# Kernel tuning notes

Measured on AMD Instinct MI355X. Metric: run time of the kernel, lower is better.

## Reference

```python
import jax, jax.numpy as jnp
import numpy as np

K = 3          # kernel size
STRIDE = 1
PAD = 1
GROUPS = 32    # GroupNorm groups
EPS = 1e-5


def setup_inputs() -> dict:
    key = jax.random.key(0)
    ks = jax.random.split(key, 6)
    B, Cin, H, W, Cout = 4, 256, 64, 64, 256
    K2 = K * K
    x = jax.random.normal(ks[0], (B, Cin, H, W), jnp.float32)
    offset = jax.random.normal(ks[1], (B, 2 * K2, H, W), jnp.float32)
    mask = jax.random.uniform(ks[2], (B, K2, H, W), jnp.float32)
    weight = jax.random.normal(ks[3], (Cout, Cin, K, K), jnp.float32) * (1.0 / np.sqrt(Cin * K2))
    bias = jnp.zeros((Cout,), jnp.float32)
    gamma = jnp.ones((Cout,), jnp.float32)   # constant_init(norm, 1)
    beta = jnp.zeros((Cout,), jnp.float32)   # bias=0
    return {"x": x, "offset": offset, "mask": mask, "weight": weight,
            "bias": bias, "gamma": gamma, "beta": beta}


def _modulated_deform_conv(x, offset, mask, weight, bias):
    """DCNv2: bilinear-sample x at learned offsets, modulate by mask, conv-accumulate."""
    B, Cin, H, W = x.shape
    Cout = weight.shape[0]
    K2 = K * K
    Ho = (H + 2 * PAD - K) // STRIDE + 1
    Wo = (W + 2 * PAD - K) // STRIDE + 1

    # base sampling grid per kernel point: [K2, Ho, Wo]
    ky, kx = jnp.meshgrid(jnp.arange(K), jnp.arange(K), indexing='ij')
    ky = ky.reshape(K2).astype(jnp.float32)
    kx = kx.reshape(K2).astype(jnp.float32)
    hs = (jnp.arange(Ho) * STRIDE - PAD).astype(jnp.float32)
    ws = (jnp.arange(Wo) * STRIDE - PAD).astype(jnp.float32)

    off = offset.reshape(B, K2, 2, Ho, Wo)  # interleaved (dy, dx) per kernel point
    y = ky[None, :, None, None] + hs[None, None, :, None] + off[:, :, 0]   # [B,K2,Ho,Wo]
    xc = kx[None, :, None, None] + ws[None, None, None, :] + off[:, :, 1]  # [B,K2,Ho,Wo]

    y0 = jnp.floor(y)
    x0 = jnp.floor(xc)
    dy = y - y0
    dx = xc - x0
    y0i = y0.astype(jnp.int32)
    x0i = x0.astype(jnp.int32)

    x_flat = x.reshape(B, Cin, H * W)

    def corner(yi, xi, w):
        # corner-wise zero padding outside the image (matches mmcv bilinear)
        valid = (yi >= 0) & (yi <= H - 1) & (xi >= 0) & (xi <= W - 1)
        idx = jnp.clip(yi, 0, H - 1) * W + jnp.clip(xi, 0, W - 1)  # [B,K2,Ho,Wo]
        idx_f = idx.reshape(B, -1)
        v = jax.vmap(lambda xf, i: xf[:, i])(x_flat, idx_f)  # [B, Cin, K2*Ho*Wo]
        wv = (w * valid.astype(w.dtype)).reshape(B, 1, -1)
        return v * wv

    val = (corner(y0i,     x0i,     (1 - dy) * (1 - dx))
         + corner(y0i,     x0i + 1, (1 - dy) * dx)
         + corner(y0i + 1, x0i,     dy * (1 - dx))
         + corner(y0i + 1, x0i + 1, dy * dx))
    val = val.reshape(B, Cin, K2, Ho, Wo) * mask[:, None]  # modulate

    w_r = weight.reshape(Cout, Cin, K2)
    out = jnp.einsum('bckhw,ock->bohw', val, w_r) + bias[None, :, None, None]
    return out


def _group_norm(x, gamma, beta):
    B, C, H, W = x.shape
    g = x.reshape(B, GROUPS, C // GROUPS, H, W)
    mu = g.mean(axis=(2, 3, 4), keepdims=True)
    var = ((g - mu) ** 2).mean(axis=(2, 3, 4), keepdims=True)
    g = (g - mu) * jax.lax.rsqrt(var + EPS)
    return g.reshape(B, C, H, W) * gamma[None, :, None, None] + beta[None, :, None, None]


def reference(x, offset, mask, weight, bias, gamma, beta):
    out = _modulated_deform_conv(x, offset, mask, weight, bias)
    out = _group_norm(out, gamma, beta)
    return jax.nn.relu(out)
```

## Files before the change

kernel.cpp:

```cpp
#include <hip/hip_runtime.h>
#include <math.h>

#define BB    4
#define CIN   256
#define HH    64
#define WWID  64
#define COUT  256
#define KKS   3
#define K2    9
#define PADV  1
#define HWSZ  4096
#define GROUPS 32
#define CPG   8
#define EPSV  1e-5f
#define NKC   36

typedef __attribute__((ext_vector_type(8))) short bf16x8;
typedef __attribute__((ext_vector_type(4))) float f32x4;
typedef __attribute__((ext_vector_type(2))) float f32x2;

__device__ __forceinline__ unsigned short f2bf(float f) {
    unsigned u = __float_as_uint(f);
    u = (u + 0x7fffu + ((u >> 16) & 1u)) >> 16;
    return (unsigned short)u;
}
__device__ __forceinline__ f32x2 up2(unsigned q) {
    f32x2 v;
    v.x = __uint_as_float(q << 16);
    v.y = __uint_as_float(q & 0xffff0000u);
    return v;
}
__device__ __forceinline__ unsigned cvtpk(f32x2 f) {
    unsigned r;
    asm("v_cvt_pk_bf16_f32 %0, %1, %2" : "=v"(r) : "v"(f.x), "v"(f.y));
    return r;
}

__global__ __launch_bounds__(256)
void k_pre(const float* __restrict__ x, unsigned short* __restrict__ xh,
           const float* __restrict__ w, unsigned short* __restrict__ wtb,
           float* __restrict__ gstat) {
    int t = threadIdx.x;
    if (blockIdx.x < 64) {
        __shared__ float tile[32][65];
        int hw0 = blockIdx.x * 64;
        int c0  = blockIdx.y * 32;
        int b   = blockIdx.z;
        const float* xp = x + (size_t)b * CIN * HWSZ;
        int col = t & 63, r0 = t >> 6;
        #pragma unroll
        for (int i = 0; i < 8; i++)
            tile[i * 4 + r0][col] = xp[(c0 + i * 4 + r0) * HWSZ + hw0 + col];
        __syncthreads();
        int hw = t >> 2, cq = t & 3;
        union { unsigned short s[8]; uint4 qq; } pk;
        #pragma unroll
        for (int k = 0; k < 8; k++) pk.s[k] = f2bf(tile[cq * 8 + k][hw]);
        *(uint4*)((char*)xh + (((size_t)b * HWSZ + hw0 + hw) * CIN + c0 + cq * 8) * 2) = pk.qq;
    } else {
        if (blockIdx.y == 0 && blockIdx.z == 0)
            for (int i = t; i < BB * GROUPS * 2 + 8; i += 256) gstat[i] = 0.f;
        int idx = (blockIdx.y * 4 + blockIdx.z) * 256 + t;
        int co = idx >> 5, c8 = idx & 31;
        int q  = c8 >> 3;
        int ks = (c8 & 7) >> 2;
        int hf = c8 & 3;
        int lane16 = hf * 16 + (co & 15);
        for (int k2 = 0; k2 < K2; k2++) {
            int kc = k2 * 4 + q;
            union { unsigned short s[8]; uint4 qq; } pk;
            #pragma unroll
            for (int j = 0; j < 8; j++)
                pk.s[j] = f2bf(w[(co * CIN + c8 * 8 + j) * K2 + k2]);
            size_t phys = (size_t)(((co >> 4) * 36 + kc)) * 2048 + ks * 1024 + lane16 * 16;
            *(uint4*)((char*)wtb + phys) = pk.qq;
        }
    }
}

#define GATHER2(garr, gwarr, kn) do { \
    int k2n_ = (kn) >> 2, qn_ = (kn) & 3; \
    int cb_ = (px0 * K2 + k2n_) * 4; \
    int4   ci_ = *(const int4*)&cidx[cb_]; \
    float4 cw_ = *(const float4*)&cwgt[cb_]; \
    gwarr[0] = cw_.x; gwarr[1] = cw_.y; gwarr[2] = cw_.z; gwarr[3] = cw_.w; \
    const char* xq_ = xb + qn_ * 128; \
    garr[0] = *(const uint4*)(xq_ + ci_.x); \
    garr[1] = *(const uint4*)(xq_ + ci_.y); \
    garr[2] = *(const uint4*)(xq_ + ci_.z); \
    garr[3] = *(const uint4*)(xq_ + ci_.w); \
} while (0)

#define ISSUE_A(Ar) do { \
    Ar[0] = *(const bf16x8*)(ap0);        Ar[1] = *(const bf16x8*)(ap0 + 1024); \
    Ar[2] = *(const bf16x8*)(ap1);        Ar[3] = *(const bf16x8*)(ap1 + 1024); \
    ap0 += 2048; ap1 += 2048; \
} while (0)

#define PACK(garr, gwarr, Bdst) do { \
    f32x2 f0 = {0.f, 0.f}, f1 = {0.f, 0.f}, f2 = {0.f, 0.f}, f3 = {0.f, 0.f}; \
    _Pragma("unroll") \
    for (int c_ = 0; c_ < 4; c_++) { \
        f32x2 wv_ = { gwarr[c_], gwarr[c_] }; \
        f0 = __builtin_elementwise_fma(wv_, up2(garr[c_].x), f0); \
        f1 = __builtin_elementwise_fma(wv_, up2(garr[c_].y), f1); \
        f2 = __builtin_elementwise_fma(wv_, up2(garr[c_].z), f2); \
        f3 = __builtin_elementwise_fma(wv_, up2(garr[c_].w), f3); \
    } \
    uint4 pk_; \
    pk_.x = cvtpk(f0); pk_.y = cvtpk(f1); pk_.z = cvtpk(f2); pk_.w = cvtpk(f3); \
    *(uint4*)&(Bdst)[bofs0] = pk_; \
} while (0)

#define MFMA_STEP(Ar, Bc) do { \
    __builtin_amdgcn_s_setprio(1); \
    _Pragma("unroll") \
    for (int ks_ = 0; ks_ < 2; ks_++) { \
        int up_ = ((ks_ * 4 + hf) ^ skey) * 8; \
        bf16x8 bv_[4]; \
        _Pragma("unroll") \
        for (int ni_ = 0; ni_ < 4; ni_++) \
            bv_[ni_] = *(const bf16x8*)&(Bc)[(ni_ * 16 + r16) * 64 + up_]; \
        _Pragma("unroll") \
        for (int mi_ = 0; mi_ < 2; mi_++) \
            _Pragma("unroll") \
            for (int ni_ = 0; ni_ < 4; ni_++) \
                acc[mi_][ni_] = __builtin_amdgcn_mfma_f32_16x16x32_bf16( \
                    Ar[mi_ * 2 + ks_], bv_[ni_], acc[mi_][ni_], 0, 0, 0); \
    } \
    __builtin_amdgcn_s_setprio(0); \
} while (0)

#define LGKM_BAR() do { \
    asm volatile("s_waitcnt lgkmcnt(0)\n\ts_barrier" ::: "memory"); \
    __builtin_amdgcn_sched_barrier(0); \
} while (0)

#define BODY(kc, Acur, Anxt, Bcur, Bnxt, gU, gwU, gF, gwF) do { \
    ISSUE_A(Anxt); \
    GATHER2(gF, gwF, (kc) + 2); \
    __builtin_amdgcn_sched_barrier(0); \
    MFMA_STEP(Acur, Bcur); \
    __builtin_amdgcn_sched_barrier(0); \
    PACK(gU, gwU, Bnxt); \
    LGKM_BAR(); \
} while (0)

__global__ __launch_bounds__(512, 2)
void k_conv(const unsigned short* __restrict__ wtb, const unsigned short* __restrict__ xh,
            const float* __restrict__ offset, const float* __restrict__ mask,
            const float* __restrict__ bias, float* __restrict__ out,
            float* __restrict__ gstat) {
    __shared__ __align__(16) unsigned short Bs[2][64 * 64];
    __shared__ __align__(16) int   cidx[64 * K2 * 4];
    __shared__ __align__(16) float cwgt[64 * K2 * 4];
    __shared__ float gs[32], gss[32];

    int lid = blockIdx.x;
    int strip = (lid & 7) * 32 + (lid >> 3);
    int b = strip >> 6;
    int hwbase = (strip & 63) * 64;

    int t = threadIdx.x, w = t >> 6, l = t & 63;
    int r16 = l & 15, hf = l >> 4;
    int skey = r16 & 7;

    if (t < 32) { gs[t] = 0.f; gss[t] = 0.f; }

    for (int i = t; i < 64 * K2; i += 512) {
        int px = i / K2, k2 = i - px * K2;
        int hw = hwbase + px;
        int ho = hw >> 6, wo = hw & 63;
        int ky = k2 / KKS, kx = k2 - ky * KKS;
        float dy = offset[((b * (2 * K2) + k2 * 2 + 0) * HWSZ) + hw];
        float dx = offset[((b * (2 * K2) + k2 * 2 + 1) * HWSZ) + hw];
        float m  = mask[(b * K2 + k2) * HWSZ + hw];
        float y  = (float)(ky + ho - PADV) + dy;
        float xc = (float)(kx + wo - PADV) + dx;
        float y0f = floorf(y), x0f = floorf(xc);
        float fy = y - y0f, fx = xc - x0f;
        int y0 = (int)y0f, x0 = (int)x0f;
        int   yy[2] = { y0, y0 + 1 };
        int   xx[2] = { x0, x0 + 1 };
        float wy[2] = { 1.f - fy, fy };
        float wx[2] = { 1.f - fx, fx };
        #pragma unroll
        for (int ii = 0; ii < 2; ii++)
            #pragma unroll
            for (int jj = 0; jj < 2; jj++) {
                int yi = yy[ii], xi = xx[jj];
                bool valid = (yi >= 0) && (yi < HH) && (xi >= 0) && (xi < WWID);
                int yc  = min(max(yi, 0), HH - 1);
                int xcc = min(max(xi, 0), WWID - 1);
                cidx[i * 4 + ii * 2 + jj] = (yc * WWID + xcc) << 9;
                cwgt[i * 4 + ii * 2 + jj] = valid ? (wy[ii] * wx[jj] * m) : 0.f;
            }
    }

    const char* wb = (const char*)wtb + (size_t)l * 16;
    const char* ap0 = wb + (size_t)((w * 2 + 0) * 36) * 2048;
    const char* ap1 = wb + (size_t)((w * 2 + 1) * 36) * 2048;

    int sc  = t & 7;
    int px0 = t >> 3;
    const char* xb = (const char*)xh + (size_t)b * HWSZ * CIN * 2 + sc * 16;
    int bofs0 = px0 * 64 + (sc ^ (px0 & 7)) * 8;

    f32x4 acc[2][4];
    #pragma unroll
    for (int mi = 0; mi < 2; mi++)
        #pragma unroll
        for (int ni = 0; ni < 4; ni++) acc[mi][ni] = (f32x4)0.f;

    __syncthreads();

    uint4 gA[4], gB[4]; float gwA[4], gwB[4];
    bf16x8 Aa[4], Ab[4];
    GATHER2(gA, gwA, 0);
    ISSUE_A(Aa);
    GATHER2(gB, gwB, 1);
    PACK(gA, gwA, Bs[0]);
    LGKM_BAR();

    unsigned short* Bs0 = &Bs[0][0];
    unsigned short* Bs1 = &Bs[1][0];

    for (int kc2 = 0; kc2 < 34; kc2 += 2) {
        BODY(kc2,     Aa, Ab, Bs0, Bs1, gB, gwB, gA, gwA);
        BODY(kc2 + 1, Ab, Aa, Bs1, Bs0, gA, gwA, gB, gwB);
    }
    ISSUE_A(Ab);
    __builtin_amdgcn_sched_barrier(0);
    MFMA_STEP(Aa, Bs0);
    __builtin_amdgcn_sched_barrier(0);
    PACK(gB, gwB, Bs1);
    LGKM_BAR();
    MFMA_STEP(Ab, Bs1);

    float s4[2] = {0,0}, ss4[2] = {0,0};
    #pragma unroll
    for (int mi = 0; mi < 2; mi++) {
        #pragma unroll
        for (int r = 0; r < 4; r++) {
            int co = w * 32 + mi * 16 + hf * 4 + r;
            float bs = bias[co];
            float* orow = out + ((size_t)(b * COUT + co)) * HWSZ;
            #pragma unroll
            for (int ni = 0; ni < 4; ni++) {
                int n = hwbase + ni * 16 + r16;
                float v = acc[mi][ni][r] + bs;
                orow[n] = v;
                s4[mi] += v; ss4[mi] += v * v;
            }
        }
    }
    int gb = hf >> 1;
    #pragma unroll
    for (int mi = 0; mi < 2; mi++) {
        atomicAdd(&gs [w * 4 + mi * 2 + gb], s4[mi]);
        atomicAdd(&gss[w * 4 + mi * 2 + gb], ss4[mi]);
    }
    __syncthreads();
    if (t < 32) {
        atomicAdd(&gstat[(b * GROUPS + t) * 2 + 0], gs[t]);
        atomicAdd(&gstat[(b * GROUPS + t) * 2 + 1], gss[t]);
    }
}

__global__ __launch_bounds__(256)
void k_gnfinal(float* __restrict__ out, const float* __restrict__ gstat,
               const float* __restrict__ gamma, const float* __restrict__ beta) {
    int i4 = blockIdx.x * 256 + threadIdx.x;
    int e  = i4 * 4;
    int c  = (e >> 12) & 255;
    int b  = e >> 20;
    int g  = c >> 3;
    float s  = gstat[((b * GROUPS) + g) * 2 + 0];
    float ss = gstat[((b * GROUPS) + g) * 2 + 1];
    const float inv = 1.f / (float)(CPG * HWSZ);
    float mu  = s * inv;
    float var = ss * inv - mu * mu;
    float rstd = rsqrtf(var + EPSV);
    float ga = gamma[c] * rstd;
    float be = beta[c] - mu * ga;
    float4 v = ((float4*)out)[i4];
    v.x = fmaxf(v.x * ga + be, 0.f);
    v.y = fmaxf(v.y * ga + be, 0.f);
    v.z = fmaxf(v.z * ga + be, 0.f);
    v.w = fmaxf(v.w * ga + be, 0.f);
    ((float4*)out)[i4] = v;
}

extern "C" void kernel_launch(void* const* d_in, const int* in_sizes, int n_in,
                              void* d_out, int out_size, void* d_ws, size_t ws_size,
                              hipStream_t stream) {
    const float* x      = (const float*)d_in[0];
    const float* offset = (const float*)d_in[1];
    const float* mask   = (const float*)d_in[2];
    const float* weight = (const float*)d_in[3];
    const float* bias   = (const float*)d_in[4];
    const float* gamma  = (const float*)d_in[5];
    const float* beta   = (const float*)d_in[6];
    float* out = (float*)d_out;

    unsigned short* xh    = (unsigned short*)d_ws;
    unsigned short* wtb   = xh + (size_t)4194304;
    float*          gstat = (float*)(wtb + (size_t)589824);

    k_pre<<<dim3(65, 8, 4), 256, 0, stream>>>(x, xh, weight, wtb, gstat);
    k_conv<<<256, 512, 0, stream>>>(wtb, xh, offset, mask, bias, out, gstat);
    k_gnfinal<<<(size_t)BB * COUT * HWSZ / 1024, 256, 0, stream>>>(out, gstat, gamma, beta);
}
```

Measured before the change: 134.4 us.

## Double K-chunk per pipeline stage to halve barriers and use nontemporal weight loads

```diff
diff --git a/kernel.cpp b/kernel.cpp
--- a/kernel.cpp
+++ b/kernel.cpp
@@ -13,7 +13,7 @@
 #define GROUPS 32
 #define CPG   8
 #define EPSV  1e-5f
-#define NKC   36
+#define NST   18
 
 typedef __attribute__((ext_vector_type(8))) short bf16x8;
 typedef __attribute__((ext_vector_type(4))) float f32x4;
@@ -91,13 +91,19 @@
     garr[3] = *(const uint4*)(xq_ + ci_.w); \
 } while (0)
 
-#define ISSUE_A(Ar) do { \
-    Ar[0] = *(const bf16x8*)(ap0);        Ar[1] = *(const bf16x8*)(ap0 + 1024); \
-    Ar[2] = *(const bf16x8*)(ap1);        Ar[3] = *(const bf16x8*)(ap1 + 1024); \
-    ap0 += 2048; ap1 += 2048; \
-} while (0)
-
-#define PACK(garr, gwarr, Bdst) do { \
+#define ISSUE_A8(Ar) do { \
+    Ar[0] = __builtin_nontemporal_load((const bf16x8*)(ap0)); \
+    Ar[1] = __builtin_nontemporal_load((const bf16x8*)(ap0 + 1024)); \
+    Ar[2] = __builtin_nontemporal_load((const bf16x8*)(ap0 + 2048)); \
+    Ar[3] = __builtin_nontemporal_load((const bf16x8*)(ap0 + 3072)); \
+    Ar[4] = __builtin_nontemporal_load((const bf16x8*)(ap1)); \
+    Ar[5] = __builtin_nontemporal_load((const bf16x8*)(ap1 + 1024)); \
+    Ar[6] = __builtin_nontemporal_load((const bf16x8*)(ap1 + 2048)); \
+    Ar[7] = __builtin_nontemporal_load((const bf16x8*)(ap1 + 3072)); \
+    ap0 += 4096; ap1 += 4096; \
+} while (0)
+
+#define PACK(garr, gwarr, Bdst, half) do { \
     f32x2 f0 = {0.f, 0.f}, f1 = {0.f, 0.f}, f2 = {0.f, 0.f}, f3 = {0.f, 0.f}; \
     _Pragma("unroll") \
     for (int c_ = 0; c_ < 4; c_++) { \
@@ -109,24 +115,24 @@
     } \
     uint4 pk_; \
     pk_.x = cvtpk(f0); pk_.y = cvtpk(f1); pk_.z = cvtpk(f2); pk_.w = cvtpk(f3); \
-    *(uint4*)&(Bdst)[bofs0] = pk_; \
+    *(uint4*)&(Bdst)[bofs0 + (half) * 64] = pk_; \
 } while (0)
 
 #define MFMA_STEP(Ar, Bc) do { \
     __builtin_amdgcn_s_setprio(1); \
     _Pragma("unroll") \
-    for (int ks_ = 0; ks_ < 2; ks_++) { \
+    for (int ks_ = 0; ks_ < 4; ks_++) { \
         int up_ = ((ks_ * 4 + hf) ^ skey) * 8; \
         bf16x8 bv_[4]; \
         _Pragma("unroll") \
         for (int ni_ = 0; ni_ < 4; ni_++) \
-            bv_[ni_] = *(const bf16x8*)&(Bc)[(ni_ * 16 + r16) * 64 + up_]; \
+            bv_[ni_] = *(const bf16x8*)&(Bc)[(ni_ * 16 + r16) * 128 + up_]; \
         _Pragma("unroll") \
         for (int mi_ = 0; mi_ < 2; mi_++) \
             _Pragma("unroll") \
             for (int ni_ = 0; ni_ < 4; ni_++) \
                 acc[mi_][ni_] = __builtin_amdgcn_mfma_f32_16x16x32_bf16( \
-                    Ar[mi_ * 2 + ks_], bv_[ni_], acc[mi_][ni_], 0, 0, 0); \
+                    Ar[mi_ * 4 + ks_], bv_[ni_], acc[mi_][ni_], 0, 0, 0); \
     } \
     __builtin_amdgcn_s_setprio(0); \
 } while (0)
@@ -136,13 +142,15 @@
     __builtin_amdgcn_sched_barrier(0); \
 } while (0)
 
-#define BODY(kc, Acur, Anxt, Bcur, Bnxt, gU, gwU, gF, gwF) do { \
-    ISSUE_A(Anxt); \
-    GATHER2(gF, gwF, (kc) + 2); \
+#define BODY(s, Acur, Anxt, Bcur, Bnxt, u0, uw0, u1, uw1, f0a, fw0, f1a, fw1) do { \
+    ISSUE_A8(Anxt); \
+    GATHER2(f0a, fw0, 2 * ((s) + 2)); \
+    GATHER2(f1a, fw1, 2 * ((s) + 2) + 1); \
     __builtin_amdgcn_sched_barrier(0); \
     MFMA_STEP(Acur, Bcur); \
     __builtin_amdgcn_sched_barrier(0); \
-    PACK(gU, gwU, Bnxt); \
+    PACK(u0, uw0, Bnxt, 0); \
+    PACK(u1, uw1, Bnxt, 1); \
     LGKM_BAR(); \
 } while (0)
 
@@ -151,7 +159,7 @@
             const float* __restrict__ offset, const float* __restrict__ mask,
             const float* __restrict__ bias, float* __restrict__ out,
             float* __restrict__ gstat) {
-    __shared__ __align__(16) unsigned short Bs[2][64 * 64];
+    __shared__ __align__(16) unsigned short Bs[2][64 * 128];
     __shared__ __align__(16) int   cidx[64 * K2 * 4];
     __shared__ __align__(16) float cwgt[64 * K2 * 4];
     __shared__ float gs[32], gss[32];
@@ -204,7 +212,7 @@
     int sc  = t & 7;
     int px0 = t >> 3;
     const char* xb = (const char*)xh + (size_t)b * HWSZ * CIN * 2 + sc * 16;
-    int bofs0 = px0 * 64 + (sc ^ (px0 & 7)) * 8;
+    int bofs0 = px0 * 128 + (sc ^ (px0 & 7)) * 8;
 
     f32x4 acc[2][4];
     #pragma unroll
@@ -214,26 +222,31 @@
 
     __syncthreads();
 
-    uint4 gA[4], gB[4]; float gwA[4], gwB[4];
-    bf16x8 Aa[4], Ab[4];
-    GATHER2(gA, gwA, 0);
-    ISSUE_A(Aa);
-    GATHER2(gB, gwB, 1);
-    PACK(gA, gwA, Bs[0]);
+    uint4 gA0[4], gA1[4], gB0[4], gB1[4];
+    float gwA0[4], gwA1[4], gwB0[4], gwB1[4];
+    bf16x8 Aa[8], Ab[8];
+    GATHER2(gA0, gwA0, 0);
+    GATHER2(gA1, gwA1, 1);
+    ISSUE_A8(Aa);
+    PACK(gA0, gwA0, Bs[0], 0);
+    PACK(gA1, gwA1, Bs[0], 1);
+    GATHER2(gB0, gwB0, 2);
+    GATHER2(gB1, gwB1, 3);
     LGKM_BAR();
 
     unsigned short* Bs0 = &Bs[0][0];
     unsigned short* Bs1 = &Bs[1][0];
 
-    for (int kc2 = 0; kc2 < 34; kc2 += 2) {
-        BODY(kc2,     Aa, Ab, Bs0, Bs1, gB, gwB, gA, gwA);
-        BODY(kc2 + 1, Ab, Aa, Bs1, Bs0, gA, gwA, gB, gwB);
-    }
-    ISSUE_A(Ab);
+    for (int s2 = 0; s2 < 16; s2 += 2) {
+        BODY(s2,     Aa, Ab, Bs0, Bs1, gB0, gwB0, gB1, gwB1, gA0, gwA0, gA1, gwA1);
+        BODY(s2 + 1, Ab, Aa, Bs1, Bs0, gA0, gwA0, gA1, gwA1, gB0, gwB0, gB1, gwB1);
+    }
+    ISSUE_A8(Ab);
     __builtin_amdgcn_sched_barrier(0);
     MFMA_STEP(Aa, Bs0);
     __builtin_amdgcn_sched_barrier(0);
-    PACK(gB, gwB, Bs1);
+    PACK(gB0, gwB0, Bs1, 0);
+    PACK(gB1, gwB1, Bs1, 1);
     LGKM_BAR();
     MFMA_STEP(Ab, Bs1);
 
```

New measurement: 142.5 us. 6.0% more time.

## Fuse GroupNorm finalize into conv kernel via cooperative grid sync

Applied to the files above, without the earlier changes.

```diff
diff --git a/kernel.cpp b/kernel.cpp
--- a/kernel.cpp
+++ b/kernel.cpp
@@ -1,5 +1,8 @@
 #include <hip/hip_runtime.h>
+#include <hip/hip_cooperative_groups.h>
 #include <math.h>
+
+namespace cg = cooperative_groups;
 
 #define BB    4
 #define CIN   256
@@ -150,11 +153,14 @@
 void k_conv(const unsigned short* __restrict__ wtb, const unsigned short* __restrict__ xh,
             const float* __restrict__ offset, const float* __restrict__ mask,
             const float* __restrict__ bias, float* __restrict__ out,
+            const float* __restrict__ gamma, const float* __restrict__ beta,
             float* __restrict__ gstat) {
     __shared__ __align__(16) unsigned short Bs[2][64 * 64];
     __shared__ __align__(16) int   cidx[64 * K2 * 4];
     __shared__ __align__(16) float cwgt[64 * K2 * 4];
     __shared__ float gs[32], gss[32];
+
+    cg::grid_group grid = cg::this_grid();
 
     int lid = blockIdx.x;
     int strip = (lid & 7) * 32 + (lid >> 3);
@@ -237,6 +243,7 @@
     LGKM_BAR();
     MFMA_STEP(Ab, Bs1);
 
+    int gb = hf >> 1;
     float s4[2] = {0,0}, ss4[2] = {0,0};
     #pragma unroll
     for (int mi = 0; mi < 2; mi++) {
@@ -244,51 +251,51 @@
         for (int r = 0; r < 4; r++) {
             int co = w * 32 + mi * 16 + hf * 4 + r;
             float bs = bias[co];
+            #pragma unroll
+            for (int ni = 0; ni < 4; ni++) {
+                float v = acc[mi][ni][r] + bs;
+                s4[mi] += v; ss4[mi] += v * v;
+            }
+        }
+    }
+    #pragma unroll
+    for (int mi = 0; mi < 2; mi++) {
+        atomicAdd(&gs [w * 4 + mi * 2 + gb], s4[mi]);
+        atomicAdd(&gss[w * 4 + mi * 2 + gb], ss4[mi]);
+    }
+    __syncthreads();
+    if (t < 32) {
+        atomicAdd(&gstat[(b * GROUPS + t) * 2 + 0], gs[t]);
+        atomicAdd(&gstat[(b * GROUPS + t) * 2 + 1], gss[t]);
+    }
+
+    __threadfence();
+    grid.sync();
+
+    const float inv = 1.f / (float)(CPG * HWSZ);
+    #pragma unroll
+    for (int mi = 0; mi < 2; mi++) {
+        int gidx = (b * GROUPS + w * 4 + mi * 2 + gb) * 2;
+        float s  = __hip_atomic_load(&gstat[gidx + 0], __ATOMIC_RELAXED, __HIP_MEMORY_SCOPE_AGENT);
+        float ss = __hip_atomic_load(&gstat[gidx + 1], __ATOMIC_RELAXED, __HIP_MEMORY_SCOPE_AGENT);
+        float mu  = s * inv;
+        float var = ss * inv - mu * mu;
+        float rstd = rsqrtf(var + EPSV);
+        #pragma unroll
+        for (int r = 0; r < 4; r++) {
+            int co = w * 32 + mi * 16 + hf * 4 + r;
+            float bs = bias[co];
+            float ga = gamma[co] * rstd;
+            float be = beta[co] - mu * ga;
             float* orow = out + ((size_t)(b * COUT + co)) * HWSZ;
             #pragma unroll
             for (int ni = 0; ni < 4; ni++) {
                 int n = hwbase + ni * 16 + r16;
                 float v = acc[mi][ni][r] + bs;
-                orow[n] = v;
-                s4[mi] += v; ss4[mi] += v * v;
+                orow[n] = fmaxf(v * ga + be, 0.f);
             }
         }
     }
-    int gb = hf >> 1;
-    #pragma unroll
-    for (int mi = 0; mi < 2; mi++) {
-        atomicAdd(&gs [w * 4 + mi * 2 + gb], s4[mi]);
-        atomicAdd(&gss[w * 4 + mi * 2 + gb], ss4[mi]);
-    }
-    __syncthreads();
-    if (t < 32) {
-        atomicAdd(&gstat[(b * GROUPS + t) * 2 + 0], gs[t]);
-        atomicAdd(&gstat[(b * GROUPS + t) * 2 + 1], gss[t]);
-    }
-}
-
-__global__ __launch_bounds__(256)
-void k_gnfinal(float* __restrict__ out, const float* __restrict__ gstat,
-               const float* __restrict__ gamma, const float* __restrict__ beta) {
-    int i4 = blockIdx.x * 256 + threadIdx.x;
-    int e  = i4 * 4;
-    int c  = (e >> 12) & 255;
-    int b  = e >> 20;
-    int g  = c >> 3;
-    float s  = gstat[((b * GROUPS) + g) * 2 + 0];
-    float ss = gstat[((b * GROUPS) + g) * 2 + 1];
-    const float inv = 1.f / (float)(CPG * HWSZ);
-    float mu  = s * inv;
-    float var = ss * inv - mu * mu;
-    float rstd = rsqrtf(var + EPSV);
-    float ga = gamma[c] * rstd;
-    float be = beta[c] - mu * ga;
-    float4 v = ((float4*)out)[i4];
-    v.x = fmaxf(v.x * ga + be, 0.f);
-    v.y = fmaxf(v.y * ga + be, 0.f);
-    v.z = fmaxf(v.z * ga + be, 0.f);
-    v.w = fmaxf(v.w * ga + be, 0.f);
-    ((float4*)out)[i4] = v;
 }
 
 extern "C" void kernel_launch(void* const* d_in, const int* in_sizes, int n_in,
@@ -308,6 +315,10 @@
     float*          gstat = (float*)(wtb + (size_t)589824);
 
     k_pre<<<dim3(65, 8, 4), 256, 0, stream>>>(x, xh, weight, wtb, gstat);
-    k_conv<<<256, 512, 0, stream>>>(wtb, xh, offset, mask, bias, out, gstat);
-    k_gnfinal<<<(size_t)BB * COUT * HWSZ / 1024, 256, 0, stream>>>(out, gstat, gamma, beta);
-}
+
+    void* params[] = { (void*)&wtb, (void*)&xh, (void*)&offset, (void*)&mask,
+                       (void*)&bias, (void*)&out, (void*)&gamma, (void*)&beta,
+                       (void*)&gstat };
+    hipLaunchCooperativeKernel(reinterpret_cast<void*>(k_conv),
+                               dim3(256), dim3(512), params, 0, stream);
+}
```

Result: slower. 217.3 us (+61.7%).
